# Performance work log

Measured on AMD Instinct MI355X. Metric: run time of the kernel, lower is better.

## Reference

```python
import jax, jax.numpy as jnp
import numpy as np
from jax import lax

IN_CH = 256
UP = 8
DN = ('NCHW', 'OIHW', 'NCHW')


def setup_inputs() -> dict:
    key = jax.random.key(0)
    ks = jax.random.split(key, 6)
    B, H, W = 8, 96, 96
    flow_lr = jax.random.normal(ks[0], (B, 2, H, W), dtype=jnp.float32)
    feat = jax.random.normal(ks[1], (B, IN_CH, H, W), dtype=jnp.float32)
    w1 = jax.random.normal(ks[2], (IN_CH, IN_CH, 3, 3), dtype=jnp.float32) * 0.02
    b1 = jnp.zeros((IN_CH,), dtype=jnp.float32)
    w2 = jax.random.normal(ks[3], (UP * UP * 9, IN_CH, 1, 1), dtype=jnp.float32) * 0.02
    b2 = jnp.zeros((UP * UP * 9,), dtype=jnp.float32)
    return {"flow_lr": flow_lr, "feat": feat, "w1": w1, "b1": b1, "w2": w2, "b2": b2}


def reference(flow_lr, feat, w1, b1, w2, b2):
    B, _, H, W = flow_lr.shape
    up = UP
    # mask head: 3x3 conv + relu + 1x1 conv
    x = lax.conv_general_dilated(feat, w1, (1, 1), 'SAME', dimension_numbers=DN)
    x = jax.nn.relu(x + b1[None, :, None, None])
    mask = lax.conv_general_dilated(x, w2, (1, 1), 'SAME', dimension_numbers=DN)
    mask = mask + b2[None, :, None, None]
    # channel dim 9*up*up splits as (9, up, up), matching torch .view(B,1,9,up,up,H,W)
    mask = mask.reshape(B, 9, up, up, H, W)
    mask = jax.nn.softmax(mask, axis=1)
    # unfold(flow_lr, 3, padding=1): 9 zero-padded 3x3 shifts, row-major (kh, kw)
    pad = jnp.pad(flow_lr, ((0, 0), (0, 0), (1, 1), (1, 1)))
    flow_unf = jnp.stack(
        [pad[:, :, i:i + H, j:j + W] for i in range(3) for j in range(3)], axis=2
    )  # (B, 2, 9, H, W)
    # convex combination over the 9 neighbors
    up_flow = jnp.einsum('bkpqhw,bckhw->bcpqhw', mask, flow_unf)  # (B,2,up,up,H,W)
    # pixel-shuffle: (B,2,p,q,H,W) -> (B,2,H,p,W,q) -> (B,2,H*up,W*up)
    up_flow = up_flow.transpose(0, 1, 4, 2, 5, 3).reshape(B, 2, H * up, W * up)
    return up_flow * up
```

## Files before the change

kernel.cpp:

```cpp
#include <hip/hip_runtime.h>
#include <hip/hip_bf16.h>
#include <stdint.h>

typedef unsigned short u16;
typedef __bf16 bf16x8 __attribute__((ext_vector_type(8)));
typedef float f32x4 __attribute__((ext_vector_type(4)));

#define MFMA16(a, b, c) __builtin_amdgcn_mfma_f32_16x16x32_bf16((a), (b), (c), 0, 0, 0)

#define GLOAD16(g, l)                                                        \
  __builtin_amdgcn_global_load_lds(                                          \
      (const __attribute__((address_space(1))) void*)(g),                    \
      (__attribute__((address_space(3))) void*)(l), 16, 0, 0)

#define SBAR() __builtin_amdgcn_s_barrier()
#define SCHEDBAR() __builtin_amdgcn_sched_barrier(0)
#define VMCNT(n) asm volatile("s_waitcnt vmcnt(" #n ")" ::: "memory")
#define LGKM0() asm volatile("s_waitcnt lgkmcnt(0)" ::: "memory")

static __device__ __forceinline__ u16 f2bf(float f) {
  union { float f; uint32_t u; } v;
  v.f = f;
  uint32_t u = v.u;
  return (u16)((u + 0x7FFFu + ((u >> 16) & 1u)) >> 16);
}
static __device__ __forceinline__ float bf2f(u16 u) {
  union { uint32_t u; float f; } v;
  v.u = ((uint32_t)u) << 16;
  return v.f;
}

#define FEATT_ELEMS (8u * 98u * 98u * 256u)
#define W1T_OFF     FEATT_ELEMS
#define W1T_ELEMS   (256u * 2304u)
#define W2B_OFF     (W1T_OFF + W1T_ELEMS)
#define W2B_ELEMS   (576u * 256u)
#define X_OFF       (W2B_OFF + W2B_ELEMS)

__global__ __launch_bounds__(256) void halo_zero(u16* __restrict__ featT) {
  int tid = blockIdx.x * 256 + threadIdx.x;
  int b = tid / (388 * 32);
  int rem = tid % (388 * 32);
  int pos = rem >> 5, v = rem & 31;
  int h, w;
  if (pos < 98) { h = 0; w = pos; }
  else if (pos < 196) { h = 97; w = pos - 98; }
  else if (pos < 292) { h = pos - 196 + 1; w = 0; }
  else { h = pos - 292 + 1; w = 97; }
  uint4* dst = (uint4*)(featT + (size_t)((b * 98 + h) * 98 + w) * 256 + v * 8);
  *dst = make_uint4(0, 0, 0, 0);
}

__global__ __launch_bounds__(256) void prep_featT(const float* __restrict__ feat,
                                                  u16* __restrict__ featT) {
  const int pt = blockIdx.x, ct = blockIdx.y, b = blockIdx.z;
  const int p0 = pt * 64, c0 = ct * 64;
  __shared__ float tile[64][65];
  const int t = threadIdx.x;
  const int pj = t & 63, ci0 = t >> 6;
#pragma unroll
  for (int r = 0; r < 16; ++r) {
    int ci = r * 4 + ci0;
    tile[ci][pj] = feat[(b * 256 + c0 + ci) * 9216 + p0 + pj];
  }
  __syncthreads();
  const int pl = t >> 2, cc0 = (t & 3) * 16;
  const int pix = p0 + pl;
  const int h = pix / 96, w = pix % 96;
  uint32_t u[8];
#pragma unroll
  for (int i = 0; i < 8; ++i) {
    u16 lo = f2bf(tile[cc0 + 2 * i][pl]);
    u16 hi = f2bf(tile[cc0 + 2 * i + 1][pl]);
    u[i] = (uint32_t)lo | ((uint32_t)hi << 16);
  }
  uint4* dst = (uint4*)(featT + (size_t)((b * 98 + h + 1) * 98 + (w + 1)) * 256 + c0 + cc0);
  dst[0] = make_uint4(u[0], u[1], u[2], u[3]);
  dst[1] = make_uint4(u[4], u[5], u[6], u[7]);
}

__global__ __launch_bounds__(256) void prep_w(const float* __restrict__ w1,
                                              const float* __restrict__ w2,
                                              u16* __restrict__ w1t,
                                              u16* __restrict__ w2b) {
  int i = blockIdx.x * 256 + threadIdx.x;
  if (i < 589824) {
    int oc = i / 2304, r = i % 2304;
    int tap = r >> 8, cin = r & 255;
    w1t[i] = f2bf(w1[(oc * 256 + cin) * 9 + tap]);
  } else {
    int j = i - 589824;
    if (j < 147456) w2b[j] = f2bf(w2[j]);
  }
}

__global__ __launch_bounds__(512, 4) void gemm1(const u16* __restrict__ featT,
                                                const u16* __restrict__ w1t,
                                                const float* __restrict__ b1,
                                                u16* __restrict__ xout) {
  __shared__ __align__(16) u16 sA[128 * 64];
  __shared__ __align__(16) u16 sB[256 * 64];
  __shared__ float sb1[256];

  const int t = threadIdx.x;
  const int wave = t >> 6, lane = t & 63;
  const int mt = blockIdx.x;
  const int b = mt / 72;
  const int ip0 = (mt % 72) * 128;

  if (t < 256) sb1[t] = b1[t];

  const u16* aBase[2];
  const u16* bBase[4];
#pragma unroll
  for (int r = 0; r < 2; ++r) {
    int row = r * 64 + wave * 8 + (lane >> 3);
    int chunk = (lane & 7) ^ (row & 7);
    int ip = ip0 + row;
    int h = ip / 96, w = ip % 96;
    aBase[r] = featT + (size_t)((b * 98 + h + 1) * 98 + (w + 1)) * 256 + chunk * 8;
  }
#pragma unroll
  for (int r = 0; r < 4; ++r) {
    int row = wave * 32 + r * 8 + (lane >> 3);
    int chunk = (lane & 7) ^ (row & 7);
    bBase[r] = w1t + (size_t)row * 2304 + chunk * 8;
  }

  const int wm = wave >> 2, wn = wave & 3;
  int aoffs[4][2], boffs[4][2];
#pragma unroll
  for (int m = 0; m < 4; ++m) {
#pragma unroll
    for (int ki = 0; ki < 2; ++ki) {
      int kc = ki * 4 + (lane >> 4);
      int rowa = wm * 64 + m * 16 + (lane & 15);
      aoffs[m][ki] = rowa * 64 + ((kc ^ (rowa & 7)) * 8);
      int rowb = wn * 64 + m * 16 + (lane & 15);
      boffs[m][ki] = rowb * 64 + ((kc ^ (rowb & 7)) * 8);
    }
  }

  f32x4 acc[4][4];
#pragma unroll
  for (int m = 0; m < 4; ++m)
#pragma unroll
    for (int n = 0; n < 4; ++n) acc[m][n] = f32x4{0.f, 0.f, 0.f, 0.f};

  for (int kt = 0; kt < 36; ++kt) {
    int tap = kt >> 2;
    int dh = tap / 3 - 1, dw = tap % 3 - 1;
    int aoff = (dh * 98 + dw) * 256 + (kt & 3) * 64;
    int boff = kt * 64;
#pragma unroll
    for (int r = 0; r < 2; ++r) GLOAD16(aBase[r] + aoff, &sA[(r * 64 + wave * 8) * 64]);
#pragma unroll
    for (int r = 0; r < 4; ++r) GLOAD16(bBase[r] + boff, &sB[(wave * 32 + r * 8) * 64]);
    __syncthreads();
#pragma unroll
    for (int ki = 0; ki < 2; ++ki) {
      bf16x8 av[4], bv[4];
#pragma unroll
      for (int m = 0; m < 4; ++m) av[m] = *(const bf16x8*)&sA[aoffs[m][ki]];
#pragma unroll
      for (int n = 0; n < 4; ++n) bv[n] = *(const bf16x8*)&sB[boffs[n][ki]];
#pragma unroll
      for (int m = 0; m < 4; ++m)
#pragma unroll
        for (int n = 0; n < 4; ++n) acc[m][n] = MFMA16(av[m], bv[n], acc[m][n]);
    }
    __syncthreads();
  }

  const int pix0g = mt * 128;
#pragma unroll
  for (int m = 0; m < 4; ++m) {
    int pixl = wm * 64 + m * 16 + ((lane >> 4) << 2);
#pragma unroll
    for (int n = 0; n < 4; ++n) {
      int oc = wn * 64 + n * 16 + (lane & 15);
      float bias = sb1[oc];
      f32x4 v = acc[m][n];
#pragma unroll
      for (int j = 0; j < 4; ++j) {
        float val = v[j] + bias;
        val = val > 0.f ? val : 0.f;
        xout[(size_t)(pix0g + pixl + j) * 256 + oc] = f2bf(val);
      }
    }
  }
}

__global__ __launch_bounds__(512, 4) void gemm2x(const u16* __restrict__ xws,
                                                 const u16* __restrict__ w2b,
                                                 const float* __restrict__ b2g,
                                                 const float* __restrict__ flow,
                                                 float* __restrict__ out) {
  __shared__ __align__(16) u16 sB2[2][18432];
  __shared__ u16 sFlowB[2304];

  const int t = threadIdx.x;
  const int wave = t >> 6, lane = t & 63;
  const int bid = blockIdx.x;
  const int mt = (bid & 7) * 72 + (bid >> 3);
  const int b = mt / 72;
  const int ipl0 = (mt % 72) * 128;
  const int l15 = lane & 15, kc = lane >> 4, g4 = kc << 2;

  for (int i = t; i < 2304; i += 512) {
    int c = i / 1152, rem = i % 1152;
    int k = rem >> 7, p = rem & 127;
    int ip = ipl0 + p;
    int h = ip / 96, w = ip % 96;
    int hh = h + k / 3 - 1, ww = w + k % 3 - 1;
    float v = 0.f;
    if (hh >= 0 && hh < 96 && ww >= 0 && ww < 96)
      v = flow[((b * 2 + c) * 96 + hh) * 96 + ww];
    sFlowB[i] = f2bf(v);
  }

  const size_t pixg = (size_t)mt * 128 + wave * 16 + l15;
  bf16x8 areg[8];
#pragma unroll
  for (int s = 0; s < 8; ++s)
    areg[s] = *(const bf16x8*)&xws[pixg * 256 + (s * 4 + kc) * 8];

  auto stageU = [&](int u, int bufi) {
    int cI = u >> 1, kh = u & 1;
#pragma unroll
    for (int pass = 0; pass < 5; ++pass) {
      if (pass < 4 || t < 256) {
        int p = pass * 512 + t;
        int n = p >> 4, cl = p & 15;
        int cg = cl ^ (n & 15);
        int chan = (n >> 4) * 64 + cI * 16 + (n & 15);
        GLOAD16(w2b + (size_t)chan * 256 + kh * 128 + cg * 8,
                &sB2[bufi][(pass * 512 + wave * 64) * 8]);
      }
    }
  };

  stageU(0, 0);
  stageU(1, 1);

  f32x4 acc2[9];
#pragma unroll
  for (int u = 0; u < 8; ++u) {
    if (u == 7) { VMCNT(0); } else { VMCNT(4); }
    SBAR(); SCHEDBAR();
    const int cI = u >> 1, kh = u & 1;
    if (kh == 0) {
#pragma unroll
      for (int nf = 0; nf < 9; ++nf) acc2[nf] = f32x4{0.f, 0.f, 0.f, 0.f};
    }
    const u16* base = sB2[u & 1];
    __builtin_amdgcn_s_setprio(1);
#pragma unroll
    for (int ki = 0; ki < 4; ++ki) {
      bf16x8 a = areg[kh * 4 + ki];
      int cc = ki * 4 + kc;
#pragma unroll
      for (int nf = 0; nf < 9; ++nf) {
        int n = nf * 16 + l15;
        bf16x8 bv = *(const bf16x8*)&base[n * 128 + ((cc ^ (n & 15)) * 8)];
        acc2[nf] = MFMA16(a, bv, acc2[nf]);
      }
    }
    __builtin_amdgcn_s_setprio(0);
    if (kh == 1) {
      int pql = l15;
      int p = cI * 2 + (pql >> 3), q = pql & 7;
#pragma unroll
      for (int j = 0; j < 4; ++j) {
        int pe = wave * 16 + g4 + j;
        float v[9], mx = -3.0e38f;
#pragma unroll
        for (int nf = 0; nf < 9; ++nf) {
          v[nf] = acc2[nf][j] + b2g[nf * 64 + cI * 16 + pql];
          mx = fmaxf(mx, v[nf]);
        }
        float ssum = 0.f, fx = 0.f, fy = 0.f;
#pragma unroll
        for (int nf = 0; nf < 9; ++nf) {
          float e = __expf(v[nf] - mx);
          ssum += e;
          fx += e * bf2f(sFlowB[nf * 128 + pe]);
          fy += e * bf2f(sFlowB[1152 + nf * 128 + pe]);
        }
        float sc = 8.0f / ssum;
        int ip = ipl0 + pe;
        int h = ip / 96, w = ip % 96;
        size_t o0 = ((size_t)(b * 2 + 0) * 768 + h * 8 + p) * 768 + w * 8 + q;
        size_t o1 = ((size_t)(b * 2 + 1) * 768 + h * 8 + p) * 768 + w * 8 + q;
        out[o0] = fx * sc;
        out[o1] = fy * sc;
      }
    }
    LGKM0();
    SBAR(); SCHEDBAR();
    if (u < 6) stageU(u + 2, u & 1);
  }
}

extern "C" void kernel_launch(void* const* d_in, const int* in_sizes, int n_in,
                              void* d_out, int out_size, void* d_ws, size_t ws_size,
                              hipStream_t stream) {
  const float* flow = (const float*)d_in[0];
  const float* feat = (const float*)d_in[1];
  const float* w1 = (const float*)d_in[2];
  const float* b1 = (const float*)d_in[3];
  const float* w2 = (const float*)d_in[4];
  const float* b2 = (const float*)d_in[5];
  float* out = (float*)d_out;
  u16* ws = (u16*)d_ws;
  u16* featT = ws;
  u16* w1t = ws + W1T_OFF;
  u16* w2b = ws + W2B_OFF;
  u16* xws = ws + X_OFF;

  halo_zero<<<388, 256, 0, stream>>>(featT);
  prep_featT<<<dim3(144, 4, 8), 256, 0, stream>>>(feat, featT);
  prep_w<<<2880, 256, 0, stream>>>(w1, w2, w1t, w2b);
  gemm1<<<576, 512, 0, stream>>>(featT, w1t, b1, xws);
  gemm2x<<<576, 512, 0, stream>>>(xws, w2b, b2, flow, out);
}
```

Measured before the change: 226.7 us.

## Transpose gemm2 MFMA operands and stage full-K weight chunks per channel group

Swaps the A/B operands of the second GEMM so each lane owns one pixel and four sub-pixel positions. Flow neighbors can then be held in registers, packed as bf16 pairs, and bias is cached in shared memory. Weights are staged as one full K=256 chunk per channel group instead of double-buffered half-K chunks, with plain __syncthreads replacing the manual vmcnt pipelining. The trade-off is less overlap between the weight loads and the MFMA work, in exchange for fewer barriers and simpler epilogue indexing with better write locality.

```diff
diff --git a/kernel.cpp b/kernel.cpp
--- a/kernel.cpp
+++ b/kernel.cpp
@@ -12,11 +12,6 @@
   __builtin_amdgcn_global_load_lds(                                          \
       (const __attribute__((address_space(1))) void*)(g),                    \
       (__attribute__((address_space(3))) void*)(l), 16, 0, 0)
-
-#define SBAR() __builtin_amdgcn_s_barrier()
-#define SCHEDBAR() __builtin_amdgcn_sched_barrier(0)
-#define VMCNT(n) asm volatile("s_waitcnt vmcnt(" #n ")" ::: "memory")
-#define LGKM0() asm volatile("s_waitcnt lgkmcnt(0)" ::: "memory")
 
 static __device__ __forceinline__ u16 f2bf(float f) {
   union { float f; uint32_t u; } v;
@@ -24,9 +19,9 @@
   uint32_t u = v.u;
   return (u16)((u + 0x7FFFu + ((u >> 16) & 1u)) >> 16);
 }
-static __device__ __forceinline__ float bf2f(u16 u) {
+static __device__ __forceinline__ float u2f(uint32_t u) {
   union { uint32_t u; float f; } v;
-  v.u = ((uint32_t)u) << 16;
+  v.u = u;
   return v.f;
 }
 
@@ -191,13 +186,14 @@
   }
 }
 
-__global__ __launch_bounds__(512, 4) void gemm2x(const u16* __restrict__ xws,
+__global__ __launch_bounds__(512, 4) void gemm2t(const u16* __restrict__ xws,
                                                  const u16* __restrict__ w2b,
                                                  const float* __restrict__ b2g,
                                                  const float* __restrict__ flow,
                                                  float* __restrict__ out) {
-  __shared__ __align__(16) u16 sB2[2][18432];
-  __shared__ u16 sFlowB[2304];
+  __shared__ __align__(16) u16 sW[36864];
+  __shared__ uint32_t sFlowP[1152];
+  __shared__ float sb2f[576];
 
   const int t = threadIdx.x;
   const int wave = t >> 6, lane = t & 63;
@@ -205,100 +201,95 @@
   const int mt = (bid & 7) * 72 + (bid >> 3);
   const int b = mt / 72;
   const int ipl0 = (mt % 72) * 128;
-  const int l15 = lane & 15, kc = lane >> 4, g4 = kc << 2;
-
-  for (int i = t; i < 2304; i += 512) {
-    int c = i / 1152, rem = i % 1152;
-    int k = rem >> 7, p = rem & 127;
+  const int l15 = lane & 15, kc = lane >> 4;
+
+  for (int i = t; i < 1152; i += 512) {
+    int nf = i >> 7, p = i & 127;
     int ip = ipl0 + p;
     int h = ip / 96, w = ip % 96;
-    int hh = h + k / 3 - 1, ww = w + k % 3 - 1;
-    float v = 0.f;
-    if (hh >= 0 && hh < 96 && ww >= 0 && ww < 96)
-      v = flow[((b * 2 + c) * 96 + hh) * 96 + ww];
-    sFlowB[i] = f2bf(v);
-  }
-
-  const size_t pixg = (size_t)mt * 128 + wave * 16 + l15;
+    int hh = h + nf / 3 - 1, ww = w + nf % 3 - 1;
+    float vx = 0.f, vy = 0.f;
+    if (hh >= 0 && hh < 96 && ww >= 0 && ww < 96) {
+      vx = flow[b * 18432 + hh * 96 + ww];
+      vy = flow[b * 18432 + 9216 + hh * 96 + ww];
+    }
+    sFlowP[i] = (uint32_t)f2bf(vx) | ((uint32_t)f2bf(vy) << 16);
+  }
+  for (int i = t; i < 576; i += 512) sb2f[i] = b2g[i];
+
+  const int pe = wave * 16 + l15;
+  const size_t pixg = (size_t)mt * 128 + pe;
   bf16x8 areg[8];
 #pragma unroll
   for (int s = 0; s < 8; ++s)
     areg[s] = *(const bf16x8*)&xws[pixg * 256 + (s * 4 + kc) * 8];
 
-  auto stageU = [&](int u, int bufi) {
-    int cI = u >> 1, kh = u & 1;
-#pragma unroll
-    for (int pass = 0; pass < 5; ++pass) {
-      if (pass < 4 || t < 256) {
-        int p = pass * 512 + t;
-        int n = p >> 4, cl = p & 15;
-        int cg = cl ^ (n & 15);
-        int chan = (n >> 4) * 64 + cI * 16 + (n & 15);
-        GLOAD16(w2b + (size_t)chan * 256 + kh * 128 + cg * 8,
-                &sB2[bufi][(pass * 512 + wave * 64) * 8]);
-      }
+  auto stageW = [&](int cI) {
+#pragma unroll
+    for (int pass = 0; pass < 9; ++pass) {
+      int c = pass * 512 + t;
+      int n = c >> 5, kl = c & 31;
+      int kg = kl ^ (n & 31);
+      int chan = (n >> 4) * 64 + cI * 16 + (n & 15);
+      GLOAD16(w2b + (size_t)chan * 256 + kg * 8, &sW[(pass * 512 + wave * 64) * 8]);
     }
   };
 
-  stageU(0, 0);
-  stageU(1, 1);
-
-  f32x4 acc2[9];
-#pragma unroll
-  for (int u = 0; u < 8; ++u) {
-    if (u == 7) { VMCNT(0); } else { VMCNT(4); }
-    SBAR(); SCHEDBAR();
-    const int cI = u >> 1, kh = u & 1;
-    if (kh == 0) {
-#pragma unroll
-      for (int nf = 0; nf < 9; ++nf) acc2[nf] = f32x4{0.f, 0.f, 0.f, 0.f};
-    }
-    const u16* base = sB2[u & 1];
+  stageW(0);
+  __syncthreads();
+
+  uint32_t fp[9];
+#pragma unroll
+  for (int nf = 0; nf < 9; ++nf) fp[nf] = sFlowP[nf * 128 + pe];
+
+  const int iph = (ipl0 + pe) / 96, ipw = (ipl0 + pe) % 96;
+  const size_t obase = ((size_t)(b * 2) * 768 + iph * 8) * 768 + ipw * 8;
+
+  for (int cI = 0; cI < 4; ++cI) {
+    f32x4 acc2[9];
+#pragma unroll
+    for (int nf = 0; nf < 9; ++nf) acc2[nf] = f32x4{0.f, 0.f, 0.f, 0.f};
     __builtin_amdgcn_s_setprio(1);
 #pragma unroll
-    for (int ki = 0; ki < 4; ++ki) {
-      bf16x8 a = areg[kh * 4 + ki];
-      int cc = ki * 4 + kc;
+    for (int ks = 0; ks < 8; ++ks) {
+      bf16x8 bx = areg[ks];
+      int klin = ks * 4 + kc;
 #pragma unroll
       for (int nf = 0; nf < 9; ++nf) {
         int n = nf * 16 + l15;
-        bf16x8 bv = *(const bf16x8*)&base[n * 128 + ((cc ^ (n & 15)) * 8)];
-        acc2[nf] = MFMA16(a, bv, acc2[nf]);
+        bf16x8 wv = *(const bf16x8*)&sW[n * 256 + ((klin ^ (n & 31)) * 8)];
+        acc2[nf] = MFMA16(wv, bx, acc2[nf]);
       }
     }
     __builtin_amdgcn_s_setprio(0);
-    if (kh == 1) {
-      int pql = l15;
+    if (cI < 3) {
+      __syncthreads();
+      stageW(cI + 1);
+    }
+#pragma unroll
+    for (int j = 0; j < 4; ++j) {
+      int pql = kc * 4 + j;
+      float v[9], mx = -3.0e38f;
+#pragma unroll
+      for (int nf = 0; nf < 9; ++nf) {
+        v[nf] = acc2[nf][j] + sb2f[nf * 64 + cI * 16 + pql];
+        mx = fmaxf(mx, v[nf]);
+      }
+      float ssum = 0.f, fx = 0.f, fy = 0.f;
+#pragma unroll
+      for (int nf = 0; nf < 9; ++nf) {
+        float e = __expf(v[nf] - mx);
+        ssum += e;
+        fx += e * u2f(fp[nf] << 16);
+        fy += e * u2f(fp[nf] & 0xFFFF0000u);
+      }
+      float sc = 8.0f / ssum;
       int p = cI * 2 + (pql >> 3), q = pql & 7;
-#pragma unroll
-      for (int j = 0; j < 4; ++j) {
-        int pe = wave * 16 + g4 + j;
-        float v[9], mx = -3.0e38f;
-#pragma unroll
-        for (int nf = 0; nf < 9; ++nf) {
-          v[nf] = acc2[nf][j] + b2g[nf * 64 + cI * 16 + pql];
-          mx = fmaxf(mx, v[nf]);
-        }
-        float ssum = 0.f, fx = 0.f, fy = 0.f;
-#pragma unroll
-        for (int nf = 0; nf < 9; ++nf) {
-          float e = __expf(v[nf] - mx);
-          ssum += e;
-          fx += e * bf2f(sFlowB[nf * 128 + pe]);
-          fy += e * bf2f(sFlowB[1152 + nf * 128 + pe]);
-        }
-        float sc = 8.0f / ssum;
-        int ip = ipl0 + pe;
-        int h = ip / 96, w = ip % 96;
-        size_t o0 = ((size_t)(b * 2 + 0) * 768 + h * 8 + p) * 768 + w * 8 + q;
-        size_t o1 = ((size_t)(b * 2 + 1) * 768 + h * 8 + p) * 768 + w * 8 + q;
-        out[o0] = fx * sc;
-        out[o1] = fy * sc;
-      }
-    }
-    LGKM0();
-    SBAR(); SCHEDBAR();
-    if (u < 6) stageU(u + 2, u & 1);
+      size_t o0 = obase + (size_t)p * 768 + q;
+      out[o0] = fx * sc;
+      out[o0 + 589824] = fy * sc;
+    }
+    if (cI < 3) __syncthreads();
   }
 }
 
@@ -322,5 +313,5 @@
   prep_featT<<<dim3(144, 4, 8), 256, 0, stream>>>(feat, featT);
   prep_w<<<2880, 256, 0, stream>>>(w1, w2, w1t, w2b);
   gemm1<<<576, 512, 0, stream>>>(featT, w1t, b1, xws);
-  gemm2x<<<576, 512, 0, stream>>>(xws, w2b, b2, flow, out);
-}
+  gemm2t<<<576, 512, 0, stream>>>(xws, w2b, b2, flow, out);
+}
```

Result: no change. 229.2 us (+1.1%).
